# Kernel optimization log

Measured on AMD Instinct MI355X. Metric: run time of the kernel, lower is better.

The kernel has to match this reference:

```python
import jax, jax.numpy as jnp
import numpy as np

N, K, H, E, HEADS, MULT = 10000, 32, 128, 128, 8, 2
HD = H // HEADS


def _ln(x, g, b):
    m = jnp.mean(x, axis=-1, keepdims=True)
    v = jnp.var(x, axis=-1, keepdims=True)
    return (x - m) * jax.lax.rsqrt(v + 1e-5) * g + b


def setup_inputs() -> dict:
    key = jax.random.key(0)
    ks = jax.random.split(key, 40)
    s = 0.05
    inp = {
        "node_features": jax.random.normal(ks[0], (N, H), jnp.float32),
        "edge_features": jax.random.normal(ks[1], (N, K, H), jnp.float32),
        "edge_attr": jax.random.normal(ks[2], (N, K, E), jnp.float32),
        "neighbor_list": jax.random.randint(ks[3], (N, K), 0, N),
        "num_valid": jax.random.randint(ks[4], (N,), 1, K + 1),
        # edge_linear: E -> H (with activation)
        "W_edge": jax.random.normal(ks[5], (E, H), jnp.float32) * s,
        "b_edge": jnp.zeros((H,), jnp.float32),
        # node_linear: 2H -> H (cat of center + gathered neighbor features)
        "W_node": jax.random.normal(ks[6], (2 * H, H), jnp.float32) * s,
        "b_node": jnp.zeros((H,), jnp.float32),
        # message_linear: 2H -> H
        "W_msg": jax.random.normal(ks[7], (2 * H, H), jnp.float32) * s,
        "b_msg": jnp.zeros((H,), jnp.float32),
        # multi-head attention in/out projections
        "W_qkv": jax.random.normal(ks[8], (H, 3 * H), jnp.float32) * s,
        "b_qkv": jnp.zeros((3 * H,), jnp.float32),
        "W_out": jax.random.normal(ks[9], (H, H), jnp.float32) * s,
        "b_out": jnp.zeros((H,), jnp.float32),
        # layernorms
        "g_attn": jnp.ones((H,), jnp.float32), "be_attn": jnp.zeros((H,), jnp.float32),
        "g_fn": jnp.ones((H,), jnp.float32), "be_fn": jnp.zeros((H,), jnp.float32),
        "g_fe": jnp.ones((H,), jnp.float32), "be_fe": jnp.zeros((H,), jnp.float32),
        # FFNs (node and edge), hidden = MULT*H
        "Wn1": jax.random.normal(ks[10], (H, MULT * H), jnp.float32) * s,
        "bn1": jnp.zeros((MULT * H,), jnp.float32),
        "Wn2": jax.random.normal(ks[11], (MULT * H, H), jnp.float32) * s,
        "bn2": jnp.zeros((H,), jnp.float32),
        "We1": jax.random.normal(ks[12], (H, MULT * H), jnp.float32) * s,
        "be1": jnp.zeros((MULT * H,), jnp.float32),
        "We2": jax.random.normal(ks[13], (MULT * H, H), jnp.float32) * s,
        "be2": jnp.zeros((H,), jnp.float32),
    }
    return inp


def _block(node_features, edge_features, edge_attr, neighbor_list, mask,
           W_edge, b_edge, W_node, b_node, W_msg, b_msg,
           W_qkv, b_qkv, W_out, b_out,
           g_attn, be_attn, g_fn, be_fn, g_fe, be_fe,
           Wn1, bn1, Wn2, bn2, We1, be1, We2, be2):
    act = jax.nn.gelu
    # --- pre-attention norm on nodes ---
    node_hidden = _ln(node_features, g_attn, be_attn)                 # [N,H]
    # --- graph attention: gather -> MLPs -> local windowed attention -> scatter ---
    edge_hidden = act(jnp.einsum('nke,eh->nkh', edge_attr, W_edge) + b_edge)   # [N,K,H]
    nbr = node_hidden[neighbor_list]                                   # [N,K,H] gather
    center = jnp.broadcast_to(node_hidden[:, None, :], nbr.shape)      # [N,K,H]
    node_cat = jnp.concatenate([center, nbr], axis=-1)                 # [N,K,2H]
    node_hid = act(jnp.einsum('nkf,fh->nkh', node_cat, W_node) + b_node)
    msg = act(jnp.einsum('nkf,fh->nkh',
                         jnp.concatenate([edge_hidden, node_hid], axis=-1),
                         W_msg) + b_msg)                               # [N,K,H]
    # multi-head self-attention per node over its K neighbors, key padding mask
    qkv = jnp.einsum('nkh,hf->nkf', msg, W_qkv) + b_qkv                # [N,K,3H]
    q, k, v = jnp.split(qkv, 3, axis=-1)
    q = q.reshape(N, K, HEADS, HD)
    k = k.reshape(N, K, HEADS, HD)
    v = v.reshape(N, K, HEADS, HD)
    scores = jnp.einsum('nqhd,nkhd->nhqk', q, k) / np.sqrt(HD)         # [N,heads,K,K]
    scores = jnp.where(mask[:, None, None, :], scores, jnp.float32(-1e9))
    attn = jax.nn.softmax(scores, axis=-1)
    ctx = jnp.einsum('nhqk,nkhd->nqhd', attn, v).reshape(N, K, H)
    edge_out = jnp.einsum('nkh,hf->nkf', ctx, W_out) + b_out           # [N,K,H]
    # masked scatter-aggregate back to nodes
    node_out = jnp.sum(edge_out * mask[:, :, None], axis=1)            # [N,H]
    # residuals
    node_features = node_out + node_features
    edge_features = edge_out + edge_features
    # --- FFN block ---
    nh = _ln(node_features, g_fn, be_fn)
    eh = _ln(edge_features, g_fe, be_fe)
    nh = act(nh @ Wn1 + bn1) @ Wn2 + bn2
    eh = jnp.einsum('nkf,fh->nkh', act(jnp.einsum('nkh,hf->nkf', eh, We1) + be1), We2) + be2
    return node_features + nh, edge_features + eh


def reference(node_features, edge_features, edge_attr, neighbor_list, num_valid,
              W_edge, b_edge, W_node, b_node, W_msg, b_msg,
              W_qkv, b_qkv, W_out, b_out,
              g_attn, be_attn, g_fn, be_fn, g_fe, be_fe,
              Wn1, bn1, Wn2, bn2, We1, be1, We2, be2):
    mask = jnp.arange(K)[None, :] < num_valid[:, None]                 # [N,K] bool
    return _block(node_features, edge_features, edge_attr, neighbor_list, mask,
                  W_edge, b_edge, W_node, b_node, W_msg, b_msg,
                  W_qkv, b_qkv, W_out, b_out,
                  g_attn, be_attn, g_fn, be_fn, g_fe, be_fe,
                  Wn1, bn1, Wn2, bn2, We1, be1, We2, be2)
```

## Files before the change

kernel.cpp:

```cpp
#include <hip/hip_runtime.h>
#include <cstddef>

#define N_NODES 10000
#define KNBR 32
#define HDIM 128
#define NHEADS 8

using short8 = __attribute__((ext_vector_type(8))) short;
using short4v = __attribute__((ext_vector_type(4))) short;
using f32x4 = __attribute__((ext_vector_type(4))) float;

__device__ __forceinline__ f32x4 mfma16(short8 a, short8 b, f32x4 c) {
  return __builtin_amdgcn_mfma_f32_16x16x32_bf16(a, b, c, 0, 0, 0);
}

__device__ __forceinline__ short f2bf(float f) {
  unsigned u = __builtin_bit_cast(unsigned, f);
  unsigned r = (u + 0x7fffu + ((u >> 16) & 1u)) >> 16;
  return (short)r;
}
__device__ __forceinline__ float bf2f(short s) {
  unsigned u = ((unsigned)(unsigned short)s) << 16;
  return __builtin_bit_cast(float, u);
}

__device__ __forceinline__ float gelu_f(float x) {
  float a = 0.7978845608028654f * fmaf(0.044715f * x, x * x, x);
  float e = __expf(2.0f * a);
  return 0.5f * x * (2.0f - 2.0f / (e + 1.0f));
}

__device__ __forceinline__ short8 ld_sw128(const short* b, int r, int ch) {
  return *(const short8*)(b + r * 128 + (((ch ^ (r & 7))) << 3));
}
__device__ __forceinline__ short8 ld_sw256(const short* b, int r, int ch) {
  return *(const short8*)(b + r * 256 + (((ch ^ (r & 7))) << 3));
}
__device__ __forceinline__ void st_sw128(short* b, int r, int col, short v) {
  b[r * 128 + ((((col >> 3) ^ (r & 7))) << 3) + (col & 7)] = v;
}
__device__ __forceinline__ void st_sw256(short* b, int r, int col, short v) {
  b[r * 256 + ((((col >> 3) ^ (r & 7))) << 3) + (col & 7)] = v;
}

template <int MT, int NT, int KS, typename ALoad, typename Epi>
__device__ __forceinline__ void wgemm(ALoad aload, const short* __restrict__ Bt,
                                      Epi epi) {
  const int lane = threadIdx.x & 63;
  const int lm = lane & 15, lq = lane >> 4;
  short8 a[MT][KS];
#pragma unroll
  for (int mt = 0; mt < MT; ++mt)
#pragma unroll
    for (int k = 0; k < KS; ++k) a[mt][k] = aload(mt * 16 + lm, k, lq);
#pragma unroll
  for (int nt = 0; nt < NT; ++nt) {
    short8 b[KS];
#pragma unroll
    for (int k = 0; k < KS; ++k)
      b[k] = *(const short8*)(Bt + (nt * 16 + lm) * (KS * 32) + k * 32 + lq * 8);
#pragma unroll
    for (int mt = 0; mt < MT; ++mt) {
      f32x4 acc = {0.f, 0.f, 0.f, 0.f};
#pragma unroll
      for (int k = 0; k < KS; ++k) acc = mfma16(a[mt][k], b[k], acc);
      epi(mt, nt, acc);
    }
  }
}

struct WSrc { const float* p[9]; };

__global__ void wprep_kernel(WSrc ws, short* __restrict__ dst) {
  const int cum[10] = {0, 16384, 49152, 81920, 131072, 147456, 180224, 212992, 245760, 278528};
  const int Ks[9] = {128, 256, 256, 128, 128, 128, 256, 128, 256};
  const int Ns[9] = {128, 128, 128, 384, 128, 256, 128, 256, 128};
  int eg = blockIdx.x * 256 + threadIdx.x;
  int id = 0;
#pragma unroll
  for (int i = 0; i < 8; ++i) id += (eg >= cum[i + 1]) ? 1 : 0;
  int e = eg - cum[id];
  int K = Ks[id];
  int n = (K == 128) ? (e >> 7) : (e >> 8);
  int k = e - n * K;
  dst[eg] = f2bf(ws.p[id][k * Ns[id] + n]);
}

__global__ __launch_bounds__(256) void ln_in_kernel(
    const float* __restrict__ in, const float* __restrict__ g,
    const float* __restrict__ be, short* __restrict__ out) {
  __shared__ float scr[32 * 8 * 2 + 64];
  const int tid = threadIdx.x;
  const int r = tid >> 3, j = tid & 7;
  const int base = blockIdx.x * 32;
  const int rg = base + r;
  const bool valid = rg < N_NODES;
  float4 v[4];
#pragma unroll
  for (int i = 0; i < 4; ++i)
    v[i] = valid ? ((const float4*)(in + (size_t)rg * 128 + j * 16))[i]
                 : make_float4(0.f, 0.f, 0.f, 0.f);
  float s = 0.f, s2 = 0.f;
#pragma unroll
  for (int i = 0; i < 4; ++i) {
    s += v[i].x + v[i].y + v[i].z + v[i].w;
    s2 = fmaf(v[i].x, v[i].x, s2); s2 = fmaf(v[i].y, v[i].y, s2);
    s2 = fmaf(v[i].z, v[i].z, s2); s2 = fmaf(v[i].w, v[i].w, s2);
  }
  scr[r * 8 + j] = s;
  scr[256 + r * 8 + j] = s2;
  __syncthreads();
  if (tid < 32) {
    float ss = 0.f, q2 = 0.f;
#pragma unroll
    for (int i = 0; i < 8; ++i) { ss += scr[tid * 8 + i]; q2 += scr[256 + tid * 8 + i]; }
    float mn = ss * (1.f / 128.f);
    float vr = fmaf(-mn, mn, q2 * (1.f / 128.f));
    scr[512 + tid] = mn;
    scr[544 + tid] = rsqrtf(vr + 1e-5f);
  }
  __syncthreads();
  if (!valid) return;
  float mn = scr[512 + r], rs = scr[544 + r];
  short8 o[2];
#pragma unroll
  for (int i = 0; i < 4; ++i) {
    int c0 = j * 16 + i * 4;
    float4 gg = *(const float4*)(g + c0);
    float4 bb = *(const float4*)(be + c0);
    float* vf = (float*)&v[i];
    float* gf = (float*)&gg;
    float* bf = (float*)&bb;
#pragma unroll
    for (int e = 0; e < 4; ++e)
      o[i >> 1][(i & 1) * 4 + e] = f2bf(fmaf((vf[e] - mn) * rs, gf[e], bf[e]));
  }
  *(short8*)(out + (size_t)rg * 128 + j * 16) = o[0];
  *(short8*)(out + (size_t)rg * 128 + j * 16 + 8) = o[1];
}

__global__ __launch_bounds__(256, 2) void egab_main(
    const float* __restrict__ nf, const float* __restrict__ ef,
    const float* __restrict__ ea, const int* __restrict__ nlist,
    const int* __restrict__ nvalid,
    const float* __restrict__ b_edge, const float* __restrict__ b_node,
    const float* __restrict__ b_msg, const float* __restrict__ b_qkv,
    const float* __restrict__ b_out, const float* __restrict__ g_fe,
    const float* __restrict__ be_fe, const float* __restrict__ be1,
    const float* __restrict__ be2,
    const short* __restrict__ WtE, const short* __restrict__ WtN,
    const short* __restrict__ WtM, const short* __restrict__ WtQ,
    const short* __restrict__ WtO, const short* __restrict__ WtE1,
    const short* __restrict__ WtE2, const short* __restrict__ nh_bf,
    float* __restrict__ out_node, float* __restrict__ out_edge) {
  __shared__ short lds[32768];
  short* R0 = lds;
  short* R1 = lds + 8192;
  short* R2 = lds + 16384;
  short* R3 = lds + 24576;

  const int tid = threadIdx.x;
  const int w = tid >> 6;
  const int lane = tid & 63;
  const int lm = lane & 15, lq = lane >> 4;
  const int base = blockIdx.x * 2;
  const int n0 = w * 32;

  {
    const float* eap = ea + (size_t)base * 4096;
    int r = tid >> 2;
    int c0 = (tid & 3) * 32;
#pragma unroll
    for (int j = 0; j < 4; ++j) {
      float4 fa = ((const float4*)eap)[tid * 8 + j * 2];
      float4 fb = ((const float4*)eap)[tid * 8 + j * 2 + 1];
      short8 v = {f2bf(fa.x), f2bf(fa.y), f2bf(fa.z), f2bf(fa.w),
                  f2bf(fb.x), f2bf(fb.y), f2bf(fb.z), f2bf(fb.w)};
      int ch = (c0 >> 3) + j;
      *(short8*)(R0 + r * 128 + ((ch ^ (r & 7)) << 3)) = v;
    }
    int rr = tid >> 2, sg = tid & 3;
    int idx = nlist[(base + (rr >> 5)) * KNBR + (rr & 31)];
    const short* srow = nh_bf + (size_t)idx * 128;
#pragma unroll
    for (int j = 0; j < 4; ++j) {
      int ch = sg * 4 + j;
      short8 v = *(const short8*)(srow + ch * 8);
      *(short8*)(R1 + rr * 128 + ((ch ^ (rr & 7)) << 3)) = v;
    }
  }
  __syncthreads();

  wgemm<4, 2, 4>(
      [&](int r, int k, int q) { return ld_sw128(R0, r, k * 4 + q); },
      WtE + (size_t)n0 * 128,
      [&](int mt, int nt, f32x4 acc) {
        int col = n0 + nt * 16 + lm;
        float bb = b_edge[col];
#pragma unroll
        for (int rr = 0; rr < 4; ++rr)
          st_sw128(R2, mt * 16 + lq * 4 + rr, col, f2bf(gelu_f(acc[rr] + bb)));
      });
  wgemm<4, 2, 8>(
      [&](int r, int k, int q) {
        if (k < 4)
          return *(const short8*)(nh_bf + (size_t)(base + (r >> 5)) * 128 +
                                  k * 32 + q * 8);
        return ld_sw128(R1, r, (k - 4) * 4 + q);
      },
      WtN + (size_t)n0 * 256,
      [&](int mt, int nt, f32x4 acc) {
        int col = n0 + nt * 16 + lm;
        float bb = b_node[col];
#pragma unroll
        for (int rr = 0; rr < 4; ++rr)
          st_sw128(R3, mt * 16 + lq * 4 + rr, col, f2bf(gelu_f(acc[rr] + bb)));
      });
  __syncthreads();

  wgemm<4, 2, 8>(
      [&](int r, int k, int q) {
        if (k < 4) return ld_sw128(R2, r, k * 4 + q);
        return ld_sw128(R3, r, (k - 4) * 4 + q);
      },
      WtM + (size_t)n0 * 256,
      [&](int mt, int nt, f32x4 acc) {
        int col = n0 + nt * 16 + lm;
        float bb = b_msg[col];
#pragma unroll
        for (int rr = 0; rr < 4; ++rr)
          st_sw128(R0, mt * 16 + lq * 4 + rr, col, f2bf(gelu_f(acc[rr] + bb)));
      });
  __syncthreads();

  {
    const int q0 = w * 96;
    wgemm<4, 6, 4>(
        [&](int r, int k, int q) { return ld_sw128(R0, r, k * 4 + q); },
        WtQ + (size_t)q0 * 128,
        [&](int mt, int nt, f32x4 acc) {
          int c = q0 + nt * 16;
          float bb = b_qkv[c + lm];
          int ni = mt >> 1;
          int m32b = (mt & 1) * 16 + lq * 4;
          if (c < 256) {
            short* dst = (c < 128 ? R1 + ((ni * 8 + (c >> 4)) * 32) * 16
                                  : R2 + ((ni * 8 + ((c - 128) >> 4)) * 32) * 16);
#pragma unroll
            for (int rr = 0; rr < 4; ++rr)
              dst[(m32b + rr) * 16 + lm] = f2bf(acc[rr] + bb);
          } else {
            int rv = (c - 256) + lm;
            short4v pv;
#pragma unroll
            for (int rr = 0; rr < 4; ++rr) pv[rr] = f2bf(acc[rr] + bb);
            int chv = m32b >> 3;
            *(short4v*)(R3 + ni * 4096 + rv * 32 + ((chv ^ (rv & 3)) << 3) +
                        (m32b & 7)) = pv;
          }
        });
  }
  __syncthreads();

  {
    const short8 zz = {0, 0, 0, 0, 0, 0, 0, 0};
    const f32x4 z4 = {0.f, 0.f, 0.f, 0.f};
#pragma unroll
    for (int it = 0; it < 4; ++it) {
      int inst = (it << 2) | w;
      int ni = inst >> 3, h = inst & 7;
      int nvv = nvalid[base + ni];
      short* qh = R1 + inst * 512;
      short* kh = R2 + inst * 512;
      short8 bk[2];
#pragma unroll
      for (int nt = 0; nt < 2; ++nt)
        bk[nt] = (lq < 2) ? *(const short8*)(kh + (nt * 16 + lm) * 16 + lq * 8) : zz;
      float sc[2][2][4];
#pragma unroll
      for (int mt = 0; mt < 2; ++mt) {
        short8 aq = (lq < 2) ? *(const short8*)(qh + (mt * 16 + lm) * 16 + lq * 8) : zz;
#pragma unroll
        for (int nt = 0; nt < 2; ++nt) {
          f32x4 s = mfma16(aq, bk[nt], z4);
#pragma unroll
          for (int rr = 0; rr < 4; ++rr) {
            float x = s[rr] * 0.25f;
            if (nt * 16 + lm >= nvv) x = -1e9f;
            sc[mt][nt][rr] = x;
          }
        }
      }
#pragma unroll
      for (int mt = 0; mt < 2; ++mt)
#pragma unroll
        for (int rr = 0; rr < 4; ++rr) {
          float x0 = sc[mt][0][rr], x1 = sc[mt][1][rr];
          float mx = fmaxf(x0, x1);
          mx = fmaxf(mx, __shfl_xor(mx, 1, 16));
          mx = fmaxf(mx, __shfl_xor(mx, 2, 16));
          mx = fmaxf(mx, __shfl_xor(mx, 4, 16));
          mx = fmaxf(mx, __shfl_xor(mx, 8, 16));
          float e0 = __expf(x0 - mx), e1 = __expf(x1 - mx);
          float sm = e0 + e1;
          sm += __shfl_xor(sm, 1, 16);
          sm += __shfl_xor(sm, 2, 16);
          sm += __shfl_xor(sm, 4, 16);
          sm += __shfl_xor(sm, 8, 16);
          float ri = 1.f / sm;
          int row = mt * 16 + lq * 4 + rr;
          qh[row * 16 + lm] = f2bf(e0 * ri);
          kh[row * 16 + lm] = f2bf(e1 * ri);
        }
#pragma unroll
      for (int mt = 0; mt < 2; ++mt) {
        const short* psrc = (lq < 2) ? qh : kh;
        short8 pa = *(const short8*)(psrc + (mt * 16 + lm) * 16 + (lq & 1) * 8);
        int rv = h * 16 + lm;
        short8 vb = *(const short8*)(R3 + ni * 4096 + rv * 32 + ((lq ^ (rv & 3)) << 3));
        f32x4 c = mfma16(pa, vb, z4);
#pragma unroll
        for (int rr = 0; rr < 4; ++rr)
          st_sw128(R0, ni * 32 + mt * 16 + lq * 4 + rr, h * 16 + lm, f2bf(c[rr]));
      }
    }
  }
  __syncthreads();

  {
    int nv0 = nvalid[base], nv1 = nvalid[base + 1];
    float nsum[2][2] = {{0.f, 0.f}, {0.f, 0.f}};
    wgemm<4, 2, 4>(
        [&](int r, int k, int q) { return ld_sw128(R0, r, k * 4 + q); },
        WtO + (size_t)n0 * 128,
        [&](int mt, int nt, f32x4 acc) {
          int col = n0 + nt * 16 + lm;
          float bb = b_out[col];
          int ni = mt >> 1;
          int nvv = ni ? nv1 : nv0;
#pragma unroll
          for (int rr = 0; rr < 4; ++rr) {
            int kk = (mt & 1) * 16 + lq * 4 + rr;
            float eo = acc[rr] + bb;
            if (kk < nvv) nsum[nt][ni] += eo;
            float efv = ef[((size_t)(base + ni) * KNBR + kk) * 128 + col];
            st_sw128(R1, mt * 16 + lq * 4 + rr, col, f2bf(eo + efv));
          }
        });
#pragma unroll
    for (int nt = 0; nt < 2; ++nt)
#pragma unroll
      for (int ni = 0; ni < 2; ++ni) {
        float v = nsum[nt][ni];
        v += __shfl_xor(v, 16, 64);
        v += __shfl_xor(v, 32, 64);
        if (lq == 0) {
          int col = n0 + nt * 16 + lm;
          out_node[(size_t)(base + ni) * 128 + col] =
              v + nf[(size_t)(base + ni) * 128 + col];
        }
      }
  }
  __syncthreads();

  {
    float* scr = (float*)R2;
    int r = tid >> 2, sg = tid & 3;
    short8 xv[4];
    float s = 0.f, s2 = 0.f;
#pragma unroll
    for (int j = 0; j < 4; ++j) {
      int ch = sg * 4 + j;
      xv[j] = *(const short8*)(R1 + r * 128 + ((ch ^ (r & 7)) << 3));
#pragma unroll
      for (int e = 0; e < 8; ++e) {
        float x = bf2f(xv[j][e]);
        s += x;
        s2 = fmaf(x, x, s2);
      }
    }
    scr[r * 4 + sg] = s;
    scr[256 + r * 4 + sg] = s2;
    __syncthreads();
    if (tid < 64) {
      float ss = scr[tid * 4] + scr[tid * 4 + 1] + scr[tid * 4 + 2] + scr[tid * 4 + 3];
      float q2 = scr[256 + tid * 4] + scr[256 + tid * 4 + 1] +
                 scr[256 + tid * 4 + 2] + scr[256 + tid * 4 + 3];
      float mn = ss * (1.f / 128.f);
      float vr = fmaf(-mn, mn, q2 * (1.f / 128.f));
      scr[512 + tid * 2] = mn;
      scr[512 + tid * 2 + 1] = rsqrtf(vr + 1e-5f);
    }
    __syncthreads();
    float mn = scr[512 + r * 2], rs = scr[512 + r * 2 + 1];
#pragma unroll
    for (int j = 0; j < 4; ++j) {
      int ch = sg * 4 + j;
      int c0 = ch * 8;
      float4 g0 = *(const float4*)(g_fe + c0);
      float4 g1 = *(const float4*)(g_fe + c0 + 4);
      float4 b0 = *(const float4*)(be_fe + c0);
      float4 b1 = *(const float4*)(be_fe + c0 + 4);
      const float* gp0 = (const float*)&g0;
      const float* gp1 = (const float*)&g1;
      const float* bp0 = (const float*)&b0;
      const float* bp1 = (const float*)&b1;
      short8 ov;
#pragma unroll
      for (int e = 0; e < 4; ++e) {
        ov[e] = f2bf(fmaf((bf2f(xv[j][e]) - mn) * rs, gp0[e], bp0[e]));
        ov[4 + e] = f2bf(fmaf((bf2f(xv[j][4 + e]) - mn) * rs, gp1[e], bp1[e]));
      }
      *(short8*)(R0 + r * 128 + ((ch ^ (r & 7)) << 3)) = ov;
    }
  }
  __syncthreads();

  {
    const int f0 = w * 64;
    wgemm<4, 4, 4>(
        [&](int r, int k, int q) { return ld_sw128(R0, r, k * 4 + q); },
        WtE1 + (size_t)f0 * 128,
        [&](int mt, int nt, f32x4 acc) {
          int col = f0 + nt * 16 + lm;
          float bb = be1[col];
#pragma unroll
          for (int rr = 0; rr < 4; ++rr)
            st_sw256(R2, mt * 16 + lq * 4 + rr, col, f2bf(gelu_f(acc[rr] + bb)));
        });
  }
  __syncthreads();

  wgemm<4, 2, 8>(
      [&](int r, int k, int q) { return ld_sw256(R2, r, k * 4 + q); },
      WtE2 + (size_t)n0 * 256,
      [&](int mt, int nt, f32x4 acc) {
        int col = n0 + nt * 16 + lm;
        float bb = be2[col];
        int ni = mt >> 1;
#pragma unroll
        for (int rr = 0; rr < 4; ++rr) {
          int m = mt * 16 + lq * 4 + rr;
          int kk = m & 31;
          float rv = bf2f(R1[m * 128 + ((((col >> 3) ^ (m & 7))) << 3) + (col & 7)]);
          out_edge[((size_t)(base + ni) * KNBR + kk) * 128 + col] = rv + acc[rr] + bb;
        }
      });
}

__global__ __launch_bounds__(256) void node_ffn_kernel(
    const float* __restrict__ nres, const float* __restrict__ g,
    const float* __restrict__ be, const short* __restrict__ WtN1,
    const float* __restrict__ bn1, const short* __restrict__ WtN2,
    const float* __restrict__ bn2, float* __restrict__ out) {
  __shared__ short lds[32768];
  short* EHN = lds;
  float* scr = (float*)(lds + 8192);
  short* HID = lds + 16384;

  const int tid = threadIdx.x;
  const int w = tid >> 6;
  const int lane = tid & 63;
  const int lm = lane & 15, lq = lane >> 4;
  const int base = blockIdx.x * 64;
  const int n0 = w * 32;

  {
    int r = tid >> 2, sg = tid & 3;
    bool valid = (base + r) < N_NODES;
    float xf[32];
#pragma unroll
    for (int i = 0; i < 8; ++i) {
      float4 v = valid ? ((const float4*)(nres + (size_t)(base + r) * 128 + sg * 32))[i]
                       : make_float4(0.f, 0.f, 0.f, 0.f);
      xf[i * 4] = v.x; xf[i * 4 + 1] = v.y; xf[i * 4 + 2] = v.z; xf[i * 4 + 3] = v.w;
    }
    float s = 0.f, s2 = 0.f;
#pragma unroll
    for (int i = 0; i < 32; ++i) { s += xf[i]; s2 = fmaf(xf[i], xf[i], s2); }
    scr[r * 4 + sg] = s;
    scr[256 + r * 4 + sg] = s2;
    __syncthreads();
    if (tid < 64) {
      float ss = scr[tid * 4] + scr[tid * 4 + 1] + scr[tid * 4 + 2] + scr[tid * 4 + 3];
      float q2 = scr[256 + tid * 4] + scr[256 + tid * 4 + 1] +
                 scr[256 + tid * 4 + 2] + scr[256 + tid * 4 + 3];
      float mn = ss * (1.f / 128.f);
      float vr = fmaf(-mn, mn, q2 * (1.f / 128.f));
      scr[512 + tid * 2] = mn;
      scr[512 + tid * 2 + 1] = rsqrtf(vr + 1e-5f);
    }
    __syncthreads();
    float mn = scr[512 + r * 2], rs = scr[512 + r * 2 + 1];
#pragma unroll
    for (int j = 0; j < 4; ++j) {
      int ch = sg * 4 + j;
      int c0 = ch * 8;
      short8 ov;
#pragma unroll
      for (int e = 0; e < 8; ++e)
        ov[e] = f2bf(fmaf((xf[j * 8 + e] - mn) * rs, g[c0 + e], be[c0 + e]));
      *(short8*)(EHN + r * 128 + ((ch ^ (r & 7)) << 3)) = ov;
    }
  }
  __syncthreads();

  {
    const int f0 = w * 64;
    wgemm<4, 4, 4>(
        [&](int r, int k, int q) { return ld_sw128(EHN, r, k * 4 + q); },
        WtN1 + (size_t)f0 * 128,
        [&](int mt, int nt, f32x4 acc) {
          int col = f0 + nt * 16 + lm;
          float bb = bn1[col];
#pragma unroll
          for (int rr = 0; rr < 4; ++rr)
            st_sw256(HID, mt * 16 + lq * 4 + rr, col, f2bf(gelu_f(acc[rr] + bb)));
        });
  }
  __syncthreads();

  wgemm<4, 2, 8>(
      [&](int r, int k, int q) { return ld_sw256(HID, r, k * 4 + q); },
      WtN2 + (size_t)n0 * 256,
      [&](int mt, int nt, f32x4 acc) {
        int col = n0 + nt * 16 + lm;
        float bb = bn2[col];
#pragma unroll
        for (int rr = 0; rr < 4; ++rr) {
          int m = mt * 16 + lq * 4 + rr;
          if (base + m < N_NODES) {
            float rv = nres[(size_t)(base + m) * 128 + col];
            out[(size_t)(base + m) * 128 + col] = rv + acc[rr] + bb;
          }
        }
      });
}

extern "C" void kernel_launch(void* const* d_in, const int* in_sizes, int n_in,
                              void* d_out, int out_size, void* d_ws,
                              size_t ws_size, hipStream_t stream) {
  (void)in_sizes; (void)n_in; (void)out_size; (void)ws_size;
  const float* nf = (const float*)d_in[0];
  const float* ef = (const float*)d_in[1];
  const float* ea = (const float*)d_in[2];
  const int* nlist = (const int*)d_in[3];
  const int* nvalid = (const int*)d_in[4];
  const float* W_edge = (const float*)d_in[5];
  const float* b_edge = (const float*)d_in[6];
  const float* W_node = (const float*)d_in[7];
  const float* b_node = (const float*)d_in[8];
  const float* W_msg = (const float*)d_in[9];
  const float* b_msg = (const float*)d_in[10];
  const float* W_qkv = (const float*)d_in[11];
  const float* b_qkv = (const float*)d_in[12];
  const float* W_out = (const float*)d_in[13];
  const float* b_out = (const float*)d_in[14];
  const float* g_attn = (const float*)d_in[15];
  const float* be_attn = (const float*)d_in[16];
  const float* g_fn = (const float*)d_in[17];
  const float* be_fn = (const float*)d_in[18];
  const float* g_fe = (const float*)d_in[19];
  const float* be_fe = (const float*)d_in[20];
  const float* Wn1 = (const float*)d_in[21];
  const float* bn1 = (const float*)d_in[22];
  const float* Wn2 = (const float*)d_in[23];
  const float* bn2 = (const float*)d_in[24];
  const float* We1 = (const float*)d_in[25];
  const float* be1 = (const float*)d_in[26];
  const float* We2 = (const float*)d_in[27];
  const float* be2 = (const float*)d_in[28];

  short* ws0 = (short*)d_ws;
  short* wsW = ws0 + 1280000;
  short* WtE = wsW;
  short* WtN = wsW + 16384;
  short* WtM = wsW + 49152;
  short* WtQ = wsW + 81920;
  short* WtO = wsW + 131072;
  short* WtE1 = wsW + 147456;
  short* WtE2 = wsW + 180224;
  short* WtN1 = wsW + 212992;
  short* WtN2 = wsW + 245760;

  float* out_node = (float*)d_out;
  float* out_edge = out_node + (size_t)N_NODES * 128;

  WSrc wsrc;
  wsrc.p[0] = W_edge; wsrc.p[1] = W_node; wsrc.p[2] = W_msg;
  wsrc.p[3] = W_qkv;  wsrc.p[4] = W_out;  wsrc.p[5] = We1;
  wsrc.p[6] = We2;    wsrc.p[7] = Wn1;    wsrc.p[8] = Wn2;

  wprep_kernel<<<1088, 256, 0, stream>>>(wsrc, wsW);
  ln_in_kernel<<<(N_NODES + 31) / 32, 256, 0, stream>>>(nf, g_attn, be_attn, ws0);
  egab_main<<<N_NODES / 2, 256, 0, stream>>>(
      nf, ef, ea, nlist, nvalid, b_edge, b_node, b_msg, b_qkv, b_out, g_fe,
      be_fe, be1, be2, WtE, WtN, WtM, WtQ, WtO, WtE1, WtE2, ws0, out_node,
      out_edge);
  node_ffn_kernel<<<(N_NODES + 63) / 64, 256, 0, stream>>>(
      out_node, g_fn, be_fn, WtN1, bn1, WtN2, bn2, out_node);
}
```

Measured before the change: 982.0 us.

## Process one node per block in main kernel and shrink node FFN tiles

```diff
diff --git a/kernel.cpp b/kernel.cpp
--- a/kernel.cpp
+++ b/kernel.cpp
@@ -139,7 +139,7 @@
   *(short8*)(out + (size_t)rg * 128 + j * 16 + 8) = o[1];
 }
 
-__global__ __launch_bounds__(256, 2) void egab_main(
+__global__ __launch_bounds__(256, 4) void egab_main(
     const float* __restrict__ nf, const float* __restrict__ ef,
     const float* __restrict__ ea, const int* __restrict__ nlist,
     const int* __restrict__ nvalid,
@@ -153,45 +153,44 @@
     const short* __restrict__ WtO, const short* __restrict__ WtE1,
     const short* __restrict__ WtE2, const short* __restrict__ nh_bf,
     float* __restrict__ out_node, float* __restrict__ out_edge) {
-  __shared__ short lds[32768];
+  __shared__ short lds[16384];
   short* R0 = lds;
-  short* R1 = lds + 8192;
-  short* R2 = lds + 16384;
-  short* R3 = lds + 24576;
+  short* R1 = lds + 4096;
+  short* R2 = lds + 8192;
+  short* R3 = lds + 12288;
 
   const int tid = threadIdx.x;
   const int w = tid >> 6;
   const int lane = tid & 63;
   const int lm = lane & 15, lq = lane >> 4;
-  const int base = blockIdx.x * 2;
+  const int base = blockIdx.x;
   const int n0 = w * 32;
 
   {
     const float* eap = ea + (size_t)base * 4096;
-    int r = tid >> 2;
-    int c0 = (tid & 3) * 32;
-#pragma unroll
-    for (int j = 0; j < 4; ++j) {
-      float4 fa = ((const float4*)eap)[tid * 8 + j * 2];
-      float4 fb = ((const float4*)eap)[tid * 8 + j * 2 + 1];
+    int r = tid >> 3;
+    int sg = tid & 7;
+#pragma unroll
+    for (int j = 0; j < 2; ++j) {
+      int ch = sg * 2 + j;
+      float4 fa = ((const float4*)eap)[r * 32 + ch * 2];
+      float4 fb = ((const float4*)eap)[r * 32 + ch * 2 + 1];
       short8 v = {f2bf(fa.x), f2bf(fa.y), f2bf(fa.z), f2bf(fa.w),
                   f2bf(fb.x), f2bf(fb.y), f2bf(fb.z), f2bf(fb.w)};
-      int ch = (c0 >> 3) + j;
       *(short8*)(R0 + r * 128 + ((ch ^ (r & 7)) << 3)) = v;
     }
-    int rr = tid >> 2, sg = tid & 3;
-    int idx = nlist[(base + (rr >> 5)) * KNBR + (rr & 31)];
+    int idx = nlist[base * KNBR + r];
     const short* srow = nh_bf + (size_t)idx * 128;
 #pragma unroll
-    for (int j = 0; j < 4; ++j) {
-      int ch = sg * 4 + j;
+    for (int j = 0; j < 2; ++j) {
+      int ch = sg * 2 + j;
       short8 v = *(const short8*)(srow + ch * 8);
-      *(short8*)(R1 + rr * 128 + ((ch ^ (rr & 7)) << 3)) = v;
-    }
-  }
-  __syncthreads();
-
-  wgemm<4, 2, 4>(
+      *(short8*)(R1 + r * 128 + ((ch ^ (r & 7)) << 3)) = v;
+    }
+  }
+  __syncthreads();
+
+  wgemm<2, 2, 4>(
       [&](int r, int k, int q) { return ld_sw128(R0, r, k * 4 + q); },
       WtE + (size_t)n0 * 128,
       [&](int mt, int nt, f32x4 acc) {
@@ -201,11 +200,10 @@
         for (int rr = 0; rr < 4; ++rr)
           st_sw128(R2, mt * 16 + lq * 4 + rr, col, f2bf(gelu_f(acc[rr] + bb)));
       });
-  wgemm<4, 2, 8>(
+  wgemm<2, 2, 8>(
       [&](int r, int k, int q) {
         if (k < 4)
-          return *(const short8*)(nh_bf + (size_t)(base + (r >> 5)) * 128 +
-                                  k * 32 + q * 8);
+          return *(const short8*)(nh_bf + (size_t)base * 128 + k * 32 + q * 8);
         return ld_sw128(R1, r, (k - 4) * 4 + q);
       },
       WtN + (size_t)n0 * 256,
@@ -218,7 +216,7 @@
       });
   __syncthreads();
 
-  wgemm<4, 2, 8>(
+  wgemm<2, 2, 8>(
       [&](int r, int k, int q) {
         if (k < 4) return ld_sw128(R2, r, k * 4 + q);
         return ld_sw128(R3, r, (k - 4) * 4 + q);
@@ -235,28 +233,26 @@
 
   {
     const int q0 = w * 96;
-    wgemm<4, 6, 4>(
+    wgemm<2, 6, 4>(
         [&](int r, int k, int q) { return ld_sw128(R0, r, k * 4 + q); },
         WtQ + (size_t)q0 * 128,
         [&](int mt, int nt, f32x4 acc) {
           int c = q0 + nt * 16;
           float bb = b_qkv[c + lm];
-          int ni = mt >> 1;
-          int m32b = (mt & 1) * 16 + lq * 4;
+          int m = mt * 16 + lq * 4;
           if (c < 256) {
-            short* dst = (c < 128 ? R1 + ((ni * 8 + (c >> 4)) * 32) * 16
-                                  : R2 + ((ni * 8 + ((c - 128) >> 4)) * 32) * 16);
+            short* dst = (c < 128 ? R1 + ((c >> 4) * 32) * 16
+                                  : R2 + (((c - 128) >> 4) * 32) * 16);
 #pragma unroll
             for (int rr = 0; rr < 4; ++rr)
-              dst[(m32b + rr) * 16 + lm] = f2bf(acc[rr] + bb);
+              dst[(m + rr) * 16 + lm] = f2bf(acc[rr] + bb);
           } else {
             int rv = (c - 256) + lm;
             short4v pv;
 #pragma unroll
             for (int rr = 0; rr < 4; ++rr) pv[rr] = f2bf(acc[rr] + bb);
-            int chv = m32b >> 3;
-            *(short4v*)(R3 + ni * 4096 + rv * 32 + ((chv ^ (rv & 3)) << 3) +
-                        (m32b & 7)) = pv;
+            int chv = m >> 3;
+            *(short4v*)(R3 + rv * 32 + ((chv ^ (rv & 3)) << 3) + (m & 7)) = pv;
           }
         });
   }
@@ -265,13 +261,12 @@
   {
     const short8 zz = {0, 0, 0, 0, 0, 0, 0, 0};
     const f32x4 z4 = {0.f, 0.f, 0.f, 0.f};
-#pragma unroll
-    for (int it = 0; it < 4; ++it) {
-      int inst = (it << 2) | w;
-      int ni = inst >> 3, h = inst & 7;
-      int nvv = nvalid[base + ni];
-      short* qh = R1 + inst * 512;
-      short* kh = R2 + inst * 512;
+    const int nvv = nvalid[base];
+#pragma unroll
+    for (int it = 0; it < 2; ++it) {
+      int h = (it << 2) | w;
+      short* qh = R1 + h * 512;
+      short* kh = R2 + h * 512;
       short8 bk[2];
 #pragma unroll
       for (int nt = 0; nt < 2; ++nt)
@@ -317,60 +312,56 @@
         const short* psrc = (lq < 2) ? qh : kh;
         short8 pa = *(const short8*)(psrc + (mt * 16 + lm) * 16 + (lq & 1) * 8);
         int rv = h * 16 + lm;
-        short8 vb = *(const short8*)(R3 + ni * 4096 + rv * 32 + ((lq ^ (rv & 3)) << 3));
+        short8 vb = *(const short8*)(R3 + rv * 32 + ((lq ^ (rv & 3)) << 3));
         f32x4 c = mfma16(pa, vb, z4);
 #pragma unroll
         for (int rr = 0; rr < 4; ++rr)
-          st_sw128(R0, ni * 32 + mt * 16 + lq * 4 + rr, h * 16 + lm, f2bf(c[rr]));
+          st_sw128(R0, mt * 16 + lq * 4 + rr, h * 16 + lm, f2bf(c[rr]));
       }
     }
   }
   __syncthreads();
 
   {
-    int nv0 = nvalid[base], nv1 = nvalid[base + 1];
-    float nsum[2][2] = {{0.f, 0.f}, {0.f, 0.f}};
-    wgemm<4, 2, 4>(
+    int nv = nvalid[base];
+    float nsum[2] = {0.f, 0.f};
+    wgemm<2, 2, 4>(
         [&](int r, int k, int q) { return ld_sw128(R0, r, k * 4 + q); },
         WtO + (size_t)n0 * 128,
         [&](int mt, int nt, f32x4 acc) {
           int col = n0 + nt * 16 + lm;
           float bb = b_out[col];
-          int ni = mt >> 1;
-          int nvv = ni ? nv1 : nv0;
 #pragma unroll
           for (int rr = 0; rr < 4; ++rr) {
-            int kk = (mt & 1) * 16 + lq * 4 + rr;
+            int kk = mt * 16 + lq * 4 + rr;
             float eo = acc[rr] + bb;
-            if (kk < nvv) nsum[nt][ni] += eo;
-            float efv = ef[((size_t)(base + ni) * KNBR + kk) * 128 + col];
-            st_sw128(R1, mt * 16 + lq * 4 + rr, col, f2bf(eo + efv));
+            if (kk < nv) nsum[nt] += eo;
+            float efv = ef[((size_t)base * KNBR + kk) * 128 + col];
+            st_sw128(R1, kk, col, f2bf(eo + efv));
           }
         });
 #pragma unroll
-    for (int nt = 0; nt < 2; ++nt)
-#pragma unroll
-      for (int ni = 0; ni < 2; ++ni) {
-        float v = nsum[nt][ni];
-        v += __shfl_xor(v, 16, 64);
-        v += __shfl_xor(v, 32, 64);
-        if (lq == 0) {
-          int col = n0 + nt * 16 + lm;
-          out_node[(size_t)(base + ni) * 128 + col] =
-              v + nf[(size_t)(base + ni) * 128 + col];
-        }
+    for (int nt = 0; nt < 2; ++nt) {
+      float v = nsum[nt];
+      v += __shfl_xor(v, 16, 64);
+      v += __shfl_xor(v, 32, 64);
+      if (lq == 0) {
+        int col = n0 + nt * 16 + lm;
+        out_node[(size_t)base * 128 + col] =
+            v + nf[(size_t)base * 128 + col];
       }
+    }
   }
   __syncthreads();
 
   {
     float* scr = (float*)R2;
-    int r = tid >> 2, sg = tid & 3;
-    short8 xv[4];
+    int r = tid >> 3, sg = tid & 7;
+    short8 xv[2];
     float s = 0.f, s2 = 0.f;
 #pragma unroll
-    for (int j = 0; j < 4; ++j) {
-      int ch = sg * 4 + j;
+    for (int j = 0; j < 2; ++j) {
+      int ch = sg * 2 + j;
       xv[j] = *(const short8*)(R1 + r * 128 + ((ch ^ (r & 7)) << 3));
 #pragma unroll
       for (int e = 0; e < 8; ++e) {
@@ -379,13 +370,13 @@
         s2 = fmaf(x, x, s2);
       }
     }
-    scr[r * 4 + sg] = s;
-    scr[256 + r * 4 + sg] = s2;
+    scr[r * 8 + sg] = s;
+    scr[256 + r * 8 + sg] = s2;
     __syncthreads();
-    if (tid < 64) {
-      float ss = scr[tid * 4] + scr[tid * 4 + 1] + scr[tid * 4 + 2] + scr[tid * 4 + 3];
-      float q2 = scr[256 + tid * 4] + scr[256 + tid * 4 + 1] +
-                 scr[256 + tid * 4 + 2] + scr[256 + tid * 4 + 3];
+    if (tid < 32) {
+      float ss = 0.f, q2 = 0.f;
+#pragma unroll
+      for (int i = 0; i < 8; ++i) { ss += scr[tid * 8 + i]; q2 += scr[256 + tid * 8 + i]; }
       float mn = ss * (1.f / 128.f);
       float vr = fmaf(-mn, mn, q2 * (1.f / 128.f));
       scr[512 + tid * 2] = mn;
@@ -394,8 +385,8 @@
     __syncthreads();
     float mn = scr[512 + r * 2], rs = scr[512 + r * 2 + 1];
 #pragma unroll
-    for (int j = 0; j < 4; ++j) {
-      int ch = sg * 4 + j;
+    for (int j = 0; j < 2; ++j) {
+      int ch = sg * 2 + j;
       int c0 = ch * 8;
       float4 g0 = *(const float4*)(g_fe + c0);
       float4 g1 = *(const float4*)(g_fe + c0 + 4);
@@ -418,7 +409,7 @@
 
   {
     const int f0 = w * 64;
-    wgemm<4, 4, 4>(
+    wgemm<2, 4, 4>(
         [&](int r, int k, int q) { return ld_sw128(R0, r, k * 4 + q); },
         WtE1 + (size_t)f0 * 128,
         [&](int mt, int nt, f32x4 acc) {
@@ -431,19 +422,17 @@
   }
   __syncthreads();
 
-  wgemm<4, 2, 8>(
+  wgemm<2, 2, 8>(
       [&](int r, int k, int q) { return ld_sw256(R2, r, k * 4 + q); },
       WtE2 + (size_t)n0 * 256,
       [&](int mt, int nt, f32x4 acc) {
         int col = n0 + nt * 16 + lm;
         float bb = be2[col];
-        int ni = mt >> 1;
 #pragma unroll
         for (int rr = 0; rr < 4; ++rr) {
           int m = mt * 16 + lq * 4 + rr;
-          int kk = m & 31;
           float rv = bf2f(R1[m * 128 + ((((col >> 3) ^ (m & 7))) << 3) + (col & 7)]);
-          out_edge[((size_t)(base + ni) * KNBR + kk) * 128 + col] = rv + acc[rr] + bb;
+          out_edge[((size_t)base * KNBR + m) * 128 + col] = rv + acc[rr] + bb;
         }
       });
 }
@@ -453,38 +442,38 @@
     const float* __restrict__ be, const short* __restrict__ WtN1,
     const float* __restrict__ bn1, const short* __restrict__ WtN2,
     const float* __restrict__ bn2, float* __restrict__ out) {
-  __shared__ short lds[32768];
+  __shared__ short lds[8192];
   short* EHN = lds;
-  float* scr = (float*)(lds + 8192);
-  short* HID = lds + 16384;
+  float* scr = (float*)(lds + 2048);
+  short* HID = lds + 4096;
 
   const int tid = threadIdx.x;
   const int w = tid >> 6;
   const int lane = tid & 63;
   const int lm = lane & 15, lq = lane >> 4;
-  const int base = blockIdx.x * 64;
+  const int base = blockIdx.x * 16;
   const int n0 = w * 32;
 
   {
-    int r = tid >> 2, sg = tid & 3;
+    int r = tid >> 4, sg = tid & 15;
     bool valid = (base + r) < N_NODES;
-    float xf[32];
-#pragma unroll
-    for (int i = 0; i < 8; ++i) {
-      float4 v = valid ? ((const float4*)(nres + (size_t)(base + r) * 128 + sg * 32))[i]
+    float xf[8];
+#pragma unroll
+    for (int i = 0; i < 2; ++i) {
+      float4 v = valid ? ((const float4*)(nres + (size_t)(base + r) * 128 + sg * 8))[i]
                        : make_float4(0.f, 0.f, 0.f, 0.f);
       xf[i * 4] = v.x; xf[i * 4 + 1] = v.y; xf[i * 4 + 2] = v.z; xf[i * 4 + 3] = v.w;
     }
     float s = 0.f, s2 = 0.f;
 #pragma unroll
-    for (int i = 0; i < 32; ++i) { s += xf[i]; s2 = fmaf(xf[i], xf[i], s2); }
-    scr[r * 4 + sg] = s;
-    scr[256 + r * 4 + sg] = s2;
+    for (int i = 0; i < 8; ++i) { s += xf[i]; s2 = fmaf(xf[i], xf[i], s2); }
+    scr[r * 16 + sg] = s;
+    scr[256 + r * 16 + sg] = s2;
     __syncthreads();
-    if (tid < 64) {
-      float ss = scr[tid * 4] + scr[tid * 4 + 1] + scr[tid * 4 + 2] + scr[tid * 4 + 3];
-      float q2 = scr[256 + tid * 4] + scr[256 + tid * 4 + 1] +
-                 scr[256 + tid * 4 + 2] + scr[256 + tid * 4 + 3];
+    if (tid < 16) {
+      float ss = 0.f, q2 = 0.f;
+#pragma unroll
+      for (int i = 0; i < 16; ++i) { ss += scr[tid * 16 + i]; q2 += scr[256 + tid * 16 + i]; }
       float mn = ss * (1.f / 128.f);
       float vr = fmaf(-mn, mn, q2 * (1.f / 128.f));
       scr[512 + tid * 2] = mn;
@@ -492,22 +481,18 @@
     }
     __syncthreads();
     float mn = scr[512 + r * 2], rs = scr[512 + r * 2 + 1];
-#pragma unroll
-    for (int j = 0; j < 4; ++j) {
-      int ch = sg * 4 + j;
-      int c0 = ch * 8;
-      short8 ov;
-#pragma unroll
-      for (int e = 0; e < 8; ++e)
-        ov[e] = f2bf(fmaf((xf[j * 8 + e] - mn) * rs, g[c0 + e], be[c0 + e]));
-      *(short8*)(EHN + r * 128 + ((ch ^ (r & 7)) << 3)) = ov;
-    }
+    int c0 = sg * 8;
+    short8 ov;
+#pragma unroll
+    for (int e = 0; e < 8; ++e)
+      ov[e] = f2bf(fmaf((xf[e] - mn) * rs, g[c0 + e], be[c0 + e]));
+    *(short8*)(EHN + r * 128 + ((sg ^ (r & 7)) << 3)) = ov;
   }
   __syncthreads();
 
   {
     const int f0 = w * 64;
-    wgemm<4, 4, 4>(
+    wgemm<1, 4, 4>(
         [&](int r, int k, int q) { return ld_sw128(EHN, r, k * 4 + q); },
         WtN1 + (size_t)f0 * 128,
         [&](int mt, int nt, f32x4 acc) {
@@ -520,7 +505,7 @@
   }
   __syncthreads();
 
-  wgemm<4, 2, 8>(
+  wgemm<1, 2, 8>(
       [&](int r, int k, int q) { return ld_sw256(HID, r, k * 4 + q); },
       WtN2 + (size_t)n0 * 256,
       [&](int mt, int nt, f32x4 acc) {
@@ -593,10 +578,10 @@
 
   wprep_kernel<<<1088, 256, 0, stream>>>(wsrc, wsW);
   ln_in_kernel<<<(N_NODES + 31) / 32, 256, 0, stream>>>(nf, g_attn, be_attn, ws0);
-  egab_main<<<N_NODES / 2, 256, 0, stream>>>(
+  egab_main<<<N_NODES, 256, 0, stream>>>(
       nf, ef, ea, nlist, nvalid, b_edge, b_node, b_msg, b_qkv, b_out, g_fe,
       be_fe, be1, be2, WtE, WtN, WtM, WtQ, WtO, WtE1, WtE2, ws0, out_node,
       out_edge);
-  node_ffn_kernel<<<(N_NODES + 63) / 64, 256, 0, stream>>>(
+  node_ffn_kernel<<<(N_NODES + 15) / 16, 256, 0, stream>>>(
       out_node, g_fn, be_fn, WtN1, bn1, WtN2, bn2, out_node);
 }
```

Result: no change. 992.6 us (+1.1%).
